# Performance work log

Measured on AMD Instinct MI355X. Metric: run time of the kernel, lower is better.

## Reference

```python
import jax, jax.numpy as jnp
import numpy as np

N = 8192
FEAT = 3
TRIG = 2
SA = 2
H = 64
ACT = 3
NEG = -1.0e9
EPS = 1e-5


def setup_inputs() -> dict:
    key = jax.random.key(0)
    ks = jax.random.split(key, 24)
    s = 0.05
    node_features = jax.random.uniform(ks[0], (N, FEAT), dtype=jnp.float32)
    adj = jax.random.randint(ks[1], (N, N), 0, 2).astype(jnp.float32)
    # ensure self-loops so every row has at least one neighbor
    adj_matrix = jnp.maximum(adj, jnp.eye(N, dtype=jnp.float32))
    trigger_context = jax.random.uniform(ks[2], (TRIG,), dtype=jnp.float32)
    sa_priors = jax.random.normal(ks[3], (N, SA), dtype=jnp.float32)
    p = lambda k, sh: jax.random.normal(k, sh, dtype=jnp.float32) * s
    return {
        "node_features": node_features,
        "adj_matrix": adj_matrix,
        "trigger_context": trigger_context,
        "sa_priors": sa_priors,
        # node_encoder: Linear(5,64) -> ReLU -> Linear(64,64)
        "w1": p(ks[4], (FEAT + TRIG, H)), "b1": jnp.zeros((H,), jnp.float32),
        "w2": p(ks[5], (H, H)), "b2": jnp.zeros((H,), jnp.float32),
        "wq": p(ks[6], (H, H)), "bq": jnp.zeros((H,), jnp.float32),
        "wk": p(ks[7], (H, H)), "bk": jnp.zeros((H,), jnp.float32),
        "wg": p(ks[8], (TRIG, H)), "bg": jnp.zeros((H,), jnp.float32),
        "stateful_bias": jnp.zeros((1,), jnp.float32),
        "wm": p(ks[9], (H, H)), "bm": jnp.zeros((H,), jnp.float32),
        "ln_g": jnp.ones((H,), jnp.float32), "ln_b": jnp.zeros((H,), jnp.float32),
        "wa1": p(ks[10], (H + SA, H)), "ba1": jnp.zeros((H,), jnp.float32),
        "wa2": p(ks[11], (H, ACT)), "ba2": jnp.zeros((ACT,), jnp.float32),
    }


def reference(node_features, adj_matrix, trigger_context, sa_priors,
              w1, b1, w2, b2, wq, bq, wk, bk, wg, bg, stateful_bias,
              wm, bm, ln_g, ln_b, wa1, ba1, wa2, ba2):
    n = node_features.shape[0]
    trig = jnp.broadcast_to(trigger_context[None, :], (n, TRIG))
    x = jnp.concatenate([node_features, trig], axis=1)          # [N, 5]
    h = jax.nn.relu(x @ w1 + b1) @ w2 + b2                       # [N, H]
    q = h @ wq + bq
    k = h @ wk + bk
    scores = (q @ k.T) * (1.0 / np.sqrt(H))                      # [N, N]
    gate_factor = jnp.mean(jax.nn.sigmoid(trigger_context @ wg + bg))
    topo = jnp.where(adj_matrix == 0, jnp.float32(NEG), adj_matrix)
    is_stateful = node_features[:, 2]
    is_reactive = 1.0 - trigger_context[0]
    sb = jnp.outer(is_stateful, is_stateful) * (stateful_bias[0] * is_reactive)
    scores = scores * gate_factor + topo + sb
    attn = jax.nn.softmax(scores, axis=1)                        # [N, N]
    messages = h @ wm + bm
    aggregated = attn @ messages                                 # [N, H]
    z = h + aggregated
    mu = jnp.mean(z, axis=-1, keepdims=True)
    var = jnp.mean(jnp.square(z - mu), axis=-1, keepdims=True)
    emb = (z - mu) * jax.lax.rsqrt(var + EPS) * ln_g + ln_b      # LayerNorm
    ai = jnp.concatenate([emb, sa_priors], axis=1)               # [N, H+2]
    q_values = jax.nn.relu(ai @ wa1 + ba1) @ wa2 + ba2           # [N, 3]
    return q_values
```

## Files before the change

kernel.cpp:

```cpp
#include <hip/hip_runtime.h>
#include <hip/hip_bf16.h>
#include <math.h>

#define N 8192
#define EPSV 1e-05f
#define NSPLIT 32
#define CPS (N / NSPLIT)
#define NSTEP (CPS / 32)

typedef short bf16x8 __attribute__((ext_vector_type(8)));
typedef float f32x4 __attribute__((ext_vector_type(4)));
typedef float f32x16 __attribute__((ext_vector_type(16)));
typedef unsigned short u16;
typedef unsigned int u32;

#define WS_SCAL 0
#define WS_H    64
#define WS_ST   (WS_H + N * 64)
#define WS_SBI  (WS_ST + N)
#define WS_DEN  (WS_SBI + N)
#define WS_AGG  (WS_DEN + N)
#define WS_F_END (WS_AGG + N * 64)
#define WU_BASE (WS_F_END * 2)
#define WU_QB (WU_BASE)
#define WU_KB (WU_BASE + N * 64)
#define WU_MB (WU_BASE + 2 * N * 64)
#define WU_MT (WU_BASE + 3 * N * 64)

static __device__ __forceinline__ u16 f2bf(float f) {
    __hip_bfloat16 h = __float2bfloat16(f);
    return *(u16*)&h;
}

__global__ void prep_k(const float* __restrict__ tc, const float* __restrict__ wg,
                       const float* __restrict__ bg, const float* __restrict__ sbias,
                       float* __restrict__ scal) {
    int j = threadIdx.x;
    float v = tc[0] * wg[j] + tc[1] * wg[64 + j] + bg[j];
    float g = 1.0f / (1.0f + __expf(-v));
    for (int off = 32; off; off >>= 1) g += __shfl_xor(g, off, 64);
    if (j == 0) {
        scal[0] = 0.125f * (g * (1.0f / 64.0f));
        scal[1] = sbias[0] * (1.0f - tc[0]);
    }
}

__global__ __launch_bounds__(256) void embed_k(
    const float* __restrict__ nf, const float* __restrict__ tc,
    const float* __restrict__ w1, const float* __restrict__ b1,
    const float* __restrict__ w2, const float* __restrict__ b2,
    const float* __restrict__ wq, const float* __restrict__ bq,
    const float* __restrict__ wk, const float* __restrict__ bk,
    const float* __restrict__ wm, const float* __restrict__ bm,
    float* __restrict__ ws)
{
    const int w = threadIdx.x >> 6, lane = threadIdx.x & 63;
    const int row = blockIdx.x * 4 + w;
    __shared__ float ts[4][64], hs[4][64];
    const float qscale = ws[WS_SCAL + 0];
    const float coef   = ws[WS_SCAL + 1];
    const float f0 = nf[row * 3], f1 = nf[row * 3 + 1], f2 = nf[row * 3 + 2];
    const float t0 = tc[0], t1 = tc[1];
    ws[WS_AGG + (size_t)row * 64 + lane] = 0.0f;
    float v = b1[lane];
    v = fmaf(f0, w1[lane], v);
    v = fmaf(f1, w1[64 + lane], v);
    v = fmaf(f2, w1[128 + lane], v);
    v = fmaf(t0, w1[192 + lane], v);
    v = fmaf(t1, w1[256 + lane], v);
    ts[w][lane] = fmaxf(v, 0.0f);
    __syncthreads();
    float hv = b2[lane];
    #pragma unroll 8
    for (int j = 0; j < 64; j++) hv = fmaf(ts[w][j], w2[j * 64 + lane], hv);
    hs[w][lane] = hv;
    ws[WS_H + row * 64 + lane] = hv;
    __syncthreads();
    float qv = bq[lane], kv = bk[lane], mv = bm[lane];
    #pragma unroll 4
    for (int j = 0; j < 64; j++) {
        const float hj = hs[w][j];
        qv = fmaf(hj, wq[j * 64 + lane], qv);
        kv = fmaf(hj, wk[j * 64 + lane], kv);
        mv = fmaf(hj, wm[j * 64 + lane], mv);
    }
    u16* wu = (u16*)ws;
    wu[WU_QB + row * 64 + lane] = f2bf(qv * qscale);
    wu[WU_KB + row * 64 + lane] = f2bf(kv);
    wu[WU_MB + row * 64 + lane] = f2bf(mv);
    if (lane == 0) {
        ws[WS_ST + row]  = f2;
        ws[WS_SBI + row] = f2 * coef;
        ws[WS_DEN + row] = 0.0f;
    }
}

__global__ __launch_bounds__(256) void transp_k(float* __restrict__ ws) {
    const u16* mb = (const u16*)ws + WU_MB;
    u16* mt = (u16*)ws + WU_MT;
    __shared__ __align__(16) u16 tile[64][72];
    const int i0 = blockIdx.x * 64;
    const int t = threadIdx.x;
    {
        const int r = t >> 2, cb = (t & 3) * 16;
        *(uint4*)&tile[r][cb]     = *(const uint4*)&mb[(size_t)(i0 + r) * 64 + cb];
        *(uint4*)&tile[r][cb + 8] = *(const uint4*)&mb[(size_t)(i0 + r) * 64 + cb + 8];
    }
    __syncthreads();
    const int c = t >> 2, rb = (t & 3) * 16;
    u16 tmp[16];
    #pragma unroll
    for (int i = 0; i < 16; i++) tmp[i] = tile[rb + i][c];
    *(uint4*)&mt[(size_t)c * N + i0 + rb]     = *(uint4*)&tmp[0];
    *(uint4*)&mt[(size_t)c * N + i0 + rb + 8] = *(uint4*)&tmp[8];
}

__global__ __launch_bounds__(256, 2) void attn_k(const float* __restrict__ adj,
                                                 float* __restrict__ ws)
{
    const int rb = blockIdx.x, sp = blockIdx.y;
    const int i0 = rb * 128, j0 = sp * CPS;
    const int tid = threadIdx.x;
    const int w = tid >> 6, lane = tid & 63;
    const int hi = lane >> 5, l31 = lane & 31;

    __shared__ __align__(16) u16 ks[256 * 64];
    __shared__ __align__(16) u16 ms[64 * 256];
    __shared__ __align__(16) u16 ps[4][32][40];
    __shared__ float stl[CPS];

    const u16* qb  = (const u16*)ws + WU_QB;
    const u16* kbp = (const u16*)ws + WU_KB;
    const u16* mtp = (const u16*)ws + WU_MT;

    #pragma unroll
    for (int i = 0; i < 8; i++) {
        const int id = tid + 256 * i;
        const int r = id >> 3, c = id & 7;
        const int off = r * 64 + (((c * 16) ^ ((r & 7) << 4)) >> 1);
        *(uint4*)&ks[off] = *(const uint4*)&kbp[(size_t)(j0 + r) * 64 + c * 8];
    }
    #pragma unroll
    for (int i = 0; i < 8; i++) {
        const int id = tid + 256 * i;
        const int r = id >> 5, c = id & 31;
        const int off = r * 256 + (((c * 16) ^ ((r & 7) << 4)) >> 1);
        *(uint4*)&ms[off] = *(const uint4*)&mtp[(size_t)r * N + j0 + c * 8];
    }
    stl[tid] = ws[WS_ST + j0 + tid];
    __syncthreads();

    const int q0 = i0 + w * 32;

    const u16* qr = qb + (size_t)(q0 + l31) * 64;
    bf16x8 qf[4];
    #pragma unroll
    for (int s = 0; s < 4; s++) qf[s] = *(const bf16x8*)&qr[s * 16 + hi * 8];

    float sbir[16];
    #pragma unroll
    for (int r = 0; r < 16; r++) {
        const int qv = (r & 3) + 8 * (r >> 2) + 4 * hi;
        sbir[r] = ws[WS_SBI + q0 + qv];
    }

    f32x16 acc[2];
    #pragma unroll
    for (int hb = 0; hb < 2; hb++)
        #pragma unroll
        for (int i = 0; i < 16; i++) acc[hb][i] = 0.0f;
    float den[16];
    #pragma unroll
    for (int r = 0; r < 16; r++) den[r] = 0.0f;

    const float* adjh = adj + (size_t)(q0 + 4 * hi) * N + j0 + l31;

    float ab[4][16];
    #pragma unroll
    for (int d = 0; d < 4; d++) {
        #pragma unroll
        for (int r = 0; r < 16; r++) {
            const int cr = (r & 3) + 8 * (r >> 2);
            ab[d][r] = adjh[(size_t)cr * N + d * 32];
        }
    }

    #pragma unroll
    for (int s = 0; s < NSTEP; s++) {
        const int loc = s * 32;
        const int cur = s & 3;

        f32x16 d;
        #pragma unroll
        for (int i = 0; i < 16; i++) d[i] = 0.0f;
        __builtin_amdgcn_s_setprio(1);
        #pragma unroll
        for (int s4 = 0; s4 < 4; s4++) {
            const int R = loc + l31;
            const bf16x8 kf = *(const bf16x8*)
                &ks[R * 64 + (((s4 * 32 + hi * 16) ^ ((R & 7) << 4)) >> 1)];
            d = __builtin_amdgcn_mfma_f32_32x32x16_bf16(qf[s4], kf, d, 0, 0, 0);
        }
        __builtin_amdgcn_s_setprio(0);

        const float stc = stl[loc + l31];
        #pragma unroll
        for (int r = 0; r < 16; r++) {
            const int qv = (r & 3) + 8 * (r >> 2) + 4 * hi;
            const float p = ab[cur][r] * __expf(fmaf(sbir[r], stc, d[r]));
            den[r] += p;
            ps[w][qv][l31] = f2bf(p);
        }

        if (s + 4 < NSTEP) {
            #pragma unroll
            for (int r = 0; r < 16; r++) {
                const int cr = (r & 3) + 8 * (r >> 2);
                ab[cur][r] = adjh[(size_t)cr * N + loc + 128];
            }
        }

        __builtin_amdgcn_s_setprio(1);
        #pragma unroll
        for (int s2 = 0; s2 < 2; s2++) {
            const bf16x8 pa = *(const bf16x8*)&ps[w][l31][s2 * 16 + hi * 8];
            #pragma unroll
            for (int hb = 0; hb < 2; hb++) {
                const int R2 = hb * 32 + l31;
                const bf16x8 mf = *(const bf16x8*)
                    &ms[R2 * 256 +
                        (((loc * 2 + s2 * 32 + hi * 16) ^ ((R2 & 7) << 4)) >> 1)];
                acc[hb] = __builtin_amdgcn_mfma_f32_32x32x16_bf16(pa, mf, acc[hb], 0, 0, 0);
            }
        }
        __builtin_amdgcn_s_setprio(0);
    }

    #pragma unroll
    for (int r = 0; r < 16; r++) {
        float dv = den[r];
        dv += __shfl_xor(dv, 1, 64);
        dv += __shfl_xor(dv, 2, 64);
        dv += __shfl_xor(dv, 4, 64);
        dv += __shfl_xor(dv, 8, 64);
        dv += __shfl_xor(dv, 16, 64);
        den[r] = dv;
    }
    if (l31 == 0) {
        #pragma unroll
        for (int r = 0; r < 16; r++) {
            const int qv = (r & 3) + 8 * (r >> 2) + 4 * hi;
            unsafeAtomicAdd(&ws[WS_DEN + q0 + qv], den[r]);
        }
    }

    float* aggp = ws + WS_AGG;
    #pragma unroll
    for (int hb = 0; hb < 2; hb++) {
        #pragma unroll
        for (int r = 0; r < 16; r++) {
            const int qv = (r & 3) + 8 * (r >> 2) + 4 * hi;
            unsafeAtomicAdd(&aggp[(size_t)(q0 + qv) * 64 + hb * 32 + l31],
                            acc[hb][r]);
        }
    }
}

__global__ __launch_bounds__(256) void final_k(
    const float* __restrict__ sa, const float* __restrict__ ln_g,
    const float* __restrict__ ln_b,
    const float* __restrict__ wa1, const float* __restrict__ ba1,
    const float* __restrict__ wa2, const float* __restrict__ ba2,
    const float* __restrict__ ws, float* __restrict__ out)
{
    const int w = threadIdx.x >> 6, lane = threadIdx.x & 63;
    const int row = blockIdx.x * 4 + w;
    __shared__ float es[4][64], hs2[4][64];
    const float a = ws[WS_AGG + (size_t)row * 64 + lane];
    const float d = ws[WS_DEN + row];
    const float z = ws[WS_H + row * 64 + lane] + a / d;
    float mu = z;
    for (int off = 32; off; off >>= 1) mu += __shfl_xor(mu, off, 64);
    mu *= (1.0f / 64.0f);
    const float zc = z - mu;
    float var = zc * zc;
    for (int off = 32; off; off >>= 1) var += __shfl_xor(var, off, 64);
    var *= (1.0f / 64.0f);
    const float emb = zc * rsqrtf(var + EPSV) * ln_g[lane] + ln_b[lane];
    es[w][lane] = emb;
    __syncthreads();
    const float sa0 = sa[row * 2], sa1 = sa[row * 2 + 1];
    float hv = ba1[lane];
    #pragma unroll 8
    for (int c = 0; c < 64; c++) hv = fmaf(es[w][c], wa1[c * 64 + lane], hv);
    hv = fmaf(sa0, wa1[64 * 64 + lane], hv);
    hv = fmaf(sa1, wa1[65 * 64 + lane], hv);
    hs2[w][lane] = fmaxf(hv, 0.0f);
    __syncthreads();
    if (lane < 3) {
        float o = ba2[lane];
        for (int u = 0; u < 64; u++) o = fmaf(hs2[w][u], wa2[u * 3 + lane], o);
        out[row * 3 + lane] = o;
    }
}

extern "C" void kernel_launch(void* const* d_in, const int* in_sizes, int n_in,
                              void* d_out, int out_size, void* d_ws, size_t ws_size,
                              hipStream_t stream)
{
    const float* nf  = (const float*)d_in[0];
    const float* adj = (const float*)d_in[1];
    const float* tc  = (const float*)d_in[2];
    const float* sa  = (const float*)d_in[3];
    const float* w1  = (const float*)d_in[4];
    const float* b1  = (const float*)d_in[5];
    const float* w2  = (const float*)d_in[6];
    const float* b2  = (const float*)d_in[7];
    const float* wq  = (const float*)d_in[8];
    const float* bq  = (const float*)d_in[9];
    const float* wk  = (const float*)d_in[10];
    const float* bk  = (const float*)d_in[11];
    const float* wg  = (const float*)d_in[12];
    const float* bg  = (const float*)d_in[13];
    const float* sb  = (const float*)d_in[14];
    const float* wm  = (const float*)d_in[15];
    const float* bm  = (const float*)d_in[16];
    const float* lng = (const float*)d_in[17];
    const float* lnb = (const float*)d_in[18];
    const float* wa1 = (const float*)d_in[19];
    const float* ba1 = (const float*)d_in[20];
    const float* wa2 = (const float*)d_in[21];
    const float* ba2 = (const float*)d_in[22];
    float* ws  = (float*)d_ws;
    float* out = (float*)d_out;

    prep_k<<<1, 64, 0, stream>>>(tc, wg, bg, sb, ws + WS_SCAL);
    embed_k<<<N / 4, 256, 0, stream>>>(nf, tc, w1, b1, w2, b2, wq, bq, wk, bk,
                                       wm, bm, ws);
    transp_k<<<N / 64, 256, 0, stream>>>(ws);
    attn_k<<<dim3(N / 128, NSPLIT), 256, 0, stream>>>(adj, ws);
    final_k<<<N / 4, 256, 0, stream>>>(sa, lng, lnb, wa1, ba1, wa2, ba2, ws, out);
}
```

Before: 450.6 us.

## Pack adjacency into LDS bitmask and keep attention probabilities in registers

The attention kernel now preloads each 256-column adjacency tile with coalesced loads and compresses it into a per-row bitmask in shared memory using wave ballots, instead of streaming fp32 adjacency values into registers inside the loop. The QK MFMA operands are swapped so each lane holds one query row, which lets the softmax numerators be packed to bf16 and exchanged across half-waves with shuffles rather than round-tripping through an LDS scratch tile. Blocks grow to 512 threads covering 256 query rows, which halves the redundant K/M tile loads per row. The denominator reduction shrinks to a single shuffle and atomic per row. In exchange, all adjacency loads now happen in a prologue that cannot overlap with MFMA work, and occupancy and register pressure change with the larger block.

```diff
diff --git a/kernel.cpp b/kernel.cpp
--- a/kernel.cpp
+++ b/kernel.cpp
@@ -13,6 +13,7 @@
 typedef float f32x16 __attribute__((ext_vector_type(16)));
 typedef unsigned short u16;
 typedef unsigned int u32;
+typedef unsigned long long u64;
 
 #define WS_SCAL 0
 #define WS_H    64
@@ -30,6 +31,14 @@
 static __device__ __forceinline__ u16 f2bf(float f) {
     __hip_bfloat16 h = __float2bfloat16(f);
     return *(u16*)&h;
+}
+static __device__ __forceinline__ u32 pk2(float a, float b) {
+    return (u32)f2bf(a) | ((u32)f2bf(b) << 16);
+}
+static __device__ __forceinline__ bf16x8 mk8(u32 a, u32 b, u32 c, u32 d) {
+    union { u32 u[4]; bf16x8 v; } x;
+    x.u[0] = a; x.u[1] = b; x.u[2] = c; x.u[3] = d;
+    return x.v;
 }
 
 __global__ void prep_k(const float* __restrict__ tc, const float* __restrict__ wg,
@@ -115,39 +124,63 @@
     *(uint4*)&mt[(size_t)c * N + i0 + rb + 8] = *(uint4*)&tmp[8];
 }
 
-__global__ __launch_bounds__(256, 2) void attn_k(const float* __restrict__ adj,
+__global__ __launch_bounds__(512, 4) void attn_k(const float* __restrict__ adj,
                                                  float* __restrict__ ws)
 {
     const int rb = blockIdx.x, sp = blockIdx.y;
-    const int i0 = rb * 128, j0 = sp * CPS;
+    const int i0 = rb * 256, j0 = sp * CPS;
     const int tid = threadIdx.x;
     const int w = tid >> 6, lane = tid & 63;
     const int hi = lane >> 5, l31 = lane & 31;
 
     __shared__ __align__(16) u16 ks[256 * 64];
     __shared__ __align__(16) u16 ms[64 * 256];
-    __shared__ __align__(16) u16 ps[4][32][40];
+    __shared__ u32 abit[256][9];
     __shared__ float stl[CPS];
 
     const u16* qb  = (const u16*)ws + WU_QB;
     const u16* kbp = (const u16*)ws + WU_KB;
     const u16* mtp = (const u16*)ws + WU_MT;
 
-    #pragma unroll
-    for (int i = 0; i < 8; i++) {
-        const int id = tid + 256 * i;
+    {
+        const size_t rowbase = (size_t)(i0 + w * 32) * N + j0;
+        #pragma unroll 2
+        for (int rb8 = 0; rb8 < 4; rb8++) {
+            float v[8][4];
+            #pragma unroll
+            for (int i = 0; i < 8; i++)
+                #pragma unroll
+                for (int g = 0; g < 4; g++)
+                    v[i][g] = adj[rowbase + (size_t)(rb8 * 8 + i) * N + g * 64 + lane];
+            #pragma unroll
+            for (int i = 0; i < 8; i++) {
+                #pragma unroll
+                for (int g = 0; g < 4; g++) {
+                    const u64 m = __ballot(v[i][g] != 0.0f);
+                    if (lane == 0) {
+                        abit[w * 32 + rb8 * 8 + i][g * 2]     = (u32)m;
+                        abit[w * 32 + rb8 * 8 + i][g * 2 + 1] = (u32)(m >> 32);
+                    }
+                }
+            }
+        }
+    }
+
+    #pragma unroll
+    for (int i = 0; i < 4; i++) {
+        const int id = tid + 512 * i;
         const int r = id >> 3, c = id & 7;
         const int off = r * 64 + (((c * 16) ^ ((r & 7) << 4)) >> 1);
         *(uint4*)&ks[off] = *(const uint4*)&kbp[(size_t)(j0 + r) * 64 + c * 8];
     }
     #pragma unroll
-    for (int i = 0; i < 8; i++) {
-        const int id = tid + 256 * i;
+    for (int i = 0; i < 4; i++) {
+        const int id = tid + 512 * i;
         const int r = id >> 5, c = id & 31;
         const int off = r * 256 + (((c * 16) ^ ((r & 7) << 4)) >> 1);
         *(uint4*)&ms[off] = *(const uint4*)&mtp[(size_t)r * N + j0 + c * 8];
     }
-    stl[tid] = ws[WS_ST + j0 + tid];
+    if (tid < 256) stl[tid] = ws[WS_ST + j0 + tid];
     __syncthreads();
 
     const int q0 = i0 + w * 32;
@@ -157,38 +190,18 @@
     #pragma unroll
     for (int s = 0; s < 4; s++) qf[s] = *(const bf16x8*)&qr[s * 16 + hi * 8];
 
-    float sbir[16];
-    #pragma unroll
-    for (int r = 0; r < 16; r++) {
-        const int qv = (r & 3) + 8 * (r >> 2) + 4 * hi;
-        sbir[r] = ws[WS_SBI + q0 + qv];
-    }
+    const float sbr = ws[WS_SBI + q0 + l31];
 
     f32x16 acc[2];
     #pragma unroll
     for (int hb = 0; hb < 2; hb++)
         #pragma unroll
         for (int i = 0; i < 16; i++) acc[hb][i] = 0.0f;
-    float den[16];
-    #pragma unroll
-    for (int r = 0; r < 16; r++) den[r] = 0.0f;
-
-    const float* adjh = adj + (size_t)(q0 + 4 * hi) * N + j0 + l31;
-
-    float ab[4][16];
-    #pragma unroll
-    for (int d = 0; d < 4; d++) {
-        #pragma unroll
-        for (int r = 0; r < 16; r++) {
-            const int cr = (r & 3) + 8 * (r >> 2);
-            ab[d][r] = adjh[(size_t)cr * N + d * 32];
-        }
-    }
+    float den = 0.0f;
 
     #pragma unroll
     for (int s = 0; s < NSTEP; s++) {
         const int loc = s * 32;
-        const int cur = s & 3;
 
         f32x16 d;
         #pragma unroll
@@ -199,60 +212,60 @@
             const int R = loc + l31;
             const bf16x8 kf = *(const bf16x8*)
                 &ks[R * 64 + (((s4 * 32 + hi * 16) ^ ((R & 7) << 4)) >> 1)];
-            d = __builtin_amdgcn_mfma_f32_32x32x16_bf16(qf[s4], kf, d, 0, 0, 0);
+            d = __builtin_amdgcn_mfma_f32_32x32x16_bf16(kf, qf[s4], d, 0, 0, 0);
         }
         __builtin_amdgcn_s_setprio(0);
 
-        const float stc = stl[loc + l31];
-        #pragma unroll
-        for (int r = 0; r < 16; r++) {
-            const int qv = (r & 3) + 8 * (r >> 2) + 4 * hi;
-            const float p = ab[cur][r] * __expf(fmaf(sbir[r], stc, d[r]));
-            den[r] += p;
-            ps[w][qv][l31] = f2bf(p);
-        }
-
-        if (s + 4 < NSTEP) {
-            #pragma unroll
-            for (int r = 0; r < 16; r++) {
-                const int cr = (r & 3) + 8 * (r >> 2);
-                ab[cur][r] = adjh[(size_t)cr * N + loc + 128];
-            }
+        const u32 wq = abit[w * 32 + l31][s] >> (4 * hi);
+
+        u32 wlo[4], whi[4];
+        #pragma unroll
+        for (int c2 = 0; c2 < 4; c2++) {
+            const f32x4 sv = *(const f32x4*)&stl[loc + c2 * 8 + hi * 4];
+            const float b0 = (float)((wq >> (8 * c2 + 0)) & 1u);
+            const float b1 = (float)((wq >> (8 * c2 + 1)) & 1u);
+            const float b2 = (float)((wq >> (8 * c2 + 2)) & 1u);
+            const float b3 = (float)((wq >> (8 * c2 + 3)) & 1u);
+            const float p0 = b0 * __expf(fmaf(sbr, sv[0], d[c2 * 4 + 0]));
+            const float p1 = b1 * __expf(fmaf(sbr, sv[1], d[c2 * 4 + 1]));
+            const float p2 = b2 * __expf(fmaf(sbr, sv[2], d[c2 * 4 + 2]));
+            const float p3 = b3 * __expf(fmaf(sbr, sv[3], d[c2 * 4 + 3]));
+            den += (p0 + p1) + (p2 + p3);
+            wlo[c2] = pk2(p0, p1);
+            whi[c2] = pk2(p2, p3);
+        }
+
+        bf16x8 pa[2];
+        #pragma unroll
+        for (int s2 = 0; s2 < 2; s2++) {
+            const u32 xl0 = (u32)__shfl_xor((int)wlo[2 * s2],     32, 64);
+            const u32 xh0 = (u32)__shfl_xor((int)whi[2 * s2],     32, 64);
+            const u32 xl1 = (u32)__shfl_xor((int)wlo[2 * s2 + 1], 32, 64);
+            const u32 xh1 = (u32)__shfl_xor((int)whi[2 * s2 + 1], 32, 64);
+            const u32 f0 = hi ? xl1 : wlo[2 * s2];
+            const u32 f1 = hi ? xh1 : whi[2 * s2];
+            const u32 f2 = hi ? wlo[2 * s2 + 1] : xl0;
+            const u32 f3 = hi ? whi[2 * s2 + 1] : xh0;
+            pa[s2] = mk8(f0, f1, f2, f3);
         }
 
         __builtin_amdgcn_s_setprio(1);
         #pragma unroll
         for (int s2 = 0; s2 < 2; s2++) {
-            const bf16x8 pa = *(const bf16x8*)&ps[w][l31][s2 * 16 + hi * 8];
             #pragma unroll
             for (int hb = 0; hb < 2; hb++) {
                 const int R2 = hb * 32 + l31;
                 const bf16x8 mf = *(const bf16x8*)
                     &ms[R2 * 256 +
                         (((loc * 2 + s2 * 32 + hi * 16) ^ ((R2 & 7) << 4)) >> 1)];
-                acc[hb] = __builtin_amdgcn_mfma_f32_32x32x16_bf16(pa, mf, acc[hb], 0, 0, 0);
+                acc[hb] = __builtin_amdgcn_mfma_f32_32x32x16_bf16(pa[s2], mf, acc[hb], 0, 0, 0);
             }
         }
         __builtin_amdgcn_s_setprio(0);
     }
 
-    #pragma unroll
-    for (int r = 0; r < 16; r++) {
-        float dv = den[r];
-        dv += __shfl_xor(dv, 1, 64);
-        dv += __shfl_xor(dv, 2, 64);
-        dv += __shfl_xor(dv, 4, 64);
-        dv += __shfl_xor(dv, 8, 64);
-        dv += __shfl_xor(dv, 16, 64);
-        den[r] = dv;
-    }
-    if (l31 == 0) {
-        #pragma unroll
-        for (int r = 0; r < 16; r++) {
-            const int qv = (r & 3) + 8 * (r >> 2) + 4 * hi;
-            unsafeAtomicAdd(&ws[WS_DEN + q0 + qv], den[r]);
-        }
-    }
+    den += __shfl_xor(den, 32, 64);
+    if (hi == 0) unsafeAtomicAdd(&ws[WS_DEN + q0 + l31], den);
 
     float* aggp = ws + WS_AGG;
     #pragma unroll
@@ -338,6 +351,6 @@
     embed_k<<<N / 4, 256, 0, stream>>>(nf, tc, w1, b1, w2, b2, wq, bq, wk, bk,
                                        wm, bm, ws);
     transp_k<<<N / 64, 256, 0, stream>>>(ws);
-    attn_k<<<dim3(N / 128, NSPLIT), 256, 0, stream>>>(adj, ws);
+    attn_k<<<dim3(N / 256, NSPLIT), 512, 0, stream>>>(adj, ws);
     final_k<<<N / 4, 256, 0, stream>>>(sa, lng, lnb, wa1, ba1, wa2, ba2, ws, out);
 }
```

Result: no change. 450.6 us (+0.0%).
